# Kernel tuning notes

Measured on AMD Instinct MI355X. Metric: run time of the kernel, lower is better.

## Reference

```python
import jax, jax.numpy as jnp
import numpy as np

EMBED_DIM = 512
NUM_HEADS = 8
HEAD_DIM = EMBED_DIM // NUM_HEADS
PAIR_DIM = 64
B, L = 2, 1024


def setup_inputs() -> dict:
    key = jax.random.key(0)
    ks = jax.random.split(key, 6)
    seq_repr = jax.random.normal(ks[0], (B, L, EMBED_DIM), dtype=jnp.float32)
    pair_repr = jax.random.normal(ks[1], (B, L, L, PAIR_DIM), dtype=jnp.float32)
    # Parameters (stored as [in, out] for x @ W)
    sc = 0.02
    W_qkv = jax.random.normal(ks[2], (EMBED_DIM, 3 * EMBED_DIM), dtype=jnp.float32) * sc
    W_bias = jax.random.normal(ks[3], (PAIR_DIM, NUM_HEADS), dtype=jnp.float32) * sc
    W_out = jax.random.normal(ks[4], (EMBED_DIM, EMBED_DIM), dtype=jnp.float32) * sc
    b_out = jax.random.normal(ks[5], (EMBED_DIM,), dtype=jnp.float32) * sc
    return {"seq_repr": seq_repr, "pair_repr": pair_repr,
            "W_qkv": W_qkv, "W_bias": W_bias, "W_out": W_out, "b_out": b_out}


def reference(seq_repr, pair_repr, W_qkv, W_bias, W_out, b_out):
    b, l, _ = seq_repr.shape
    # pair bias: [B, L, L, pair_dim] -> [B, H, L, L]
    pair_bias = jnp.einsum('bijp,ph->bhij', pair_repr, W_bias)
    qkv = seq_repr @ W_qkv                      # [B, L, 3*E]
    q, k, v = jnp.split(qkv, 3, axis=-1)
    def heads(x):
        return x.reshape(b, l, NUM_HEADS, HEAD_DIM).transpose(0, 2, 1, 3)  # [B,H,L,D]
    q, k, v = heads(q), heads(k), heads(v)
    scale = 1.0 / jnp.sqrt(jnp.asarray(HEAD_DIM, dtype=q.dtype))
    scores = jnp.einsum('bhid,bhjd->bhij', q, k) * scale + pair_bias
    attn = jax.nn.softmax(scores, axis=-1)
    ctx = jnp.einsum('bhij,bhjd->bhid', attn, v)             # [B,H,L,D]
    ctx = ctx.transpose(0, 2, 1, 3).reshape(b, l, EMBED_DIM)
    return ctx @ W_out + b_out
```

## Files before the change

kernel.cpp:

```cpp
#include <hip/hip_runtime.h>
#include <hip/hip_bf16.h>


typedef __attribute__((ext_vector_type(8))) short bf16x8;
typedef __attribute__((ext_vector_type(4))) float f32x4;

#define BFLO(u) __uint_as_float(((unsigned)(u)) << 16)

__device__ __forceinline__ unsigned pk2(float a, float b) {
    __hip_bfloat16 ha = __float2bfloat16(a);
    __hip_bfloat16 hb = __float2bfloat16(b);
    return (unsigned)__bfloat16_as_ushort(ha) | ((unsigned)__bfloat16_as_ushort(hb) << 16);
}

__device__ __forceinline__ void gl16_nt(const void* g, void* l) {
    __builtin_amdgcn_global_load_lds((const __attribute__((address_space(1))) void*)g,
                                     (__attribute__((address_space(3))) void*)l, 16, 0, 2);
}

__global__ __launch_bounds__(256) void prep_kernel(
    const float* __restrict__ seq, const float* __restrict__ W,
    unsigned short* __restrict__ seqb, unsigned short* __restrict__ wtb)
{
    __shared__ float T[64 * 68];
    const int bx = blockIdx.x, t = threadIdx.x;
    if (bx < 512) {
        const size_t idx = ((size_t)bx * 256 + t) * 8;
        float4 f0 = *(const float4*)&seq[idx];
        float4 f1 = *(const float4*)&seq[idx + 4];
        uint4 u;
        u.x = pk2(f0.x, f0.y); u.y = pk2(f0.z, f0.w);
        u.z = pk2(f1.x, f1.y); u.w = pk2(f1.z, f1.w);
        *(uint4*)&seqb[idx] = u;
    } else {
        const int bb = bx - 512;
        const int n0 = (bb % 24) * 64, k0 = (bb / 24) * 64;
        const int kk = t >> 2, nch = (t & 3) * 16;
#pragma unroll
        for (int u = 0; u < 4; u++) {
            float4 f = *(const float4*)&W[(size_t)(k0 + kk) * 1536 + n0 + nch + u * 4];
            T[kk * 68 + nch + u * 4 + 0] = f.x;
            T[kk * 68 + nch + u * 4 + 1] = f.y;
            T[kk * 68 + nch + u * 4 + 2] = f.z;
            T[kk * 68 + nch + u * 4 + 3] = f.w;
        }
        __syncthreads();
        const int nn = t >> 2, kch = (t & 3) * 16;
#pragma unroll
        for (int u = 0; u < 4; u++) {
            float a = T[(kch + u * 4 + 0) * 68 + nn];
            float b = T[(kch + u * 4 + 1) * 68 + nn];
            float c = T[(kch + u * 4 + 2) * 68 + nn];
            float d = T[(kch + u * 4 + 3) * 68 + nn];
            uint2 p; p.x = pk2(a, b); p.y = pk2(c, d);
            *(uint2*)&wtb[(size_t)(n0 + nn) * 512 + k0 + kch + u * 4] = p;
        }
    }
}

__global__ __launch_bounds__(256) void gemm_qkv_kernel(
    const unsigned short* __restrict__ seqb, const unsigned short* __restrict__ wtb,
    unsigned short* __restrict__ qbus, unsigned short* __restrict__ kbus,
    unsigned short* __restrict__ vtbus)
{
    const int t    = threadIdx.x;
    const int lane = t & 63;
    const int wv   = t >> 6;
    const int q4   = lane >> 4;
    const int l15  = lane & 15;
    const int mw   = wv >> 1, nw = wv & 1;

    const int m0 = blockIdx.y * 64;
    const int n0 = blockIdx.x * 64;

    f32x4 acc[2][2];
#pragma unroll
    for (int a = 0; a < 2; a++)
#pragma unroll
        for (int b = 0; b < 2; b++) acc[a][b] = (f32x4){0.f, 0.f, 0.f, 0.f};

    const unsigned short* arow0 = seqb + (size_t)(m0 + mw * 32 + l15) * 512 + q4 * 8;
    const unsigned short* brow0 = wtb + (size_t)(n0 + nw * 32 + l15) * 512 + q4 * 8;

#pragma unroll 4
    for (int k0 = 0; k0 < 512; k0 += 32) {
        uint4 af[2], bf[2];
        af[0] = *(const uint4*)(arow0 + k0);
        af[1] = *(const uint4*)(arow0 + 16 * 512 + k0);
        bf[0] = *(const uint4*)(brow0 + k0);
        bf[1] = *(const uint4*)(brow0 + 16 * 512 + k0);
#pragma unroll
        for (int sm = 0; sm < 2; sm++)
#pragma unroll
            for (int sn = 0; sn < 2; sn++)
                acc[sm][sn] = __builtin_amdgcn_mfma_f32_16x16x32_bf16(
                    *(bf16x8*)&af[sm], *(bf16x8*)&bf[sn], acc[sm][sn], 0, 0, 0);
    }

    const int sect = n0 >> 9;
    const int h    = (n0 >> 6) & 7;
    const int b    = m0 >> 10;
    const int i0   = m0 & 1023;

#pragma unroll
    for (int sm = 0; sm < 2; sm++) {
#pragma unroll
        for (int sn = 0; sn < 2; sn++) {
            const int d  = nw * 32 + sn * 16 + l15;
            const int ib = i0 + mw * 32 + sm * 16 + q4 * 4;
            if (sect == 2) {
                uint2 p;
                p.x = pk2(acc[sm][sn][0], acc[sm][sn][1]);
                p.y = pk2(acc[sm][sn][2], acc[sm][sn][3]);
                *(uint2*)&vtbus[(((size_t)(b * 8 + h)) * 64 + d) * 1024 + ib] = p;
            } else {
                unsigned short* dst = (sect == 0) ? qbus : kbus;
                const float sc = (sect == 0) ? 0.125f : 1.0f;
#pragma unroll
                for (int rr = 0; rr < 4; rr++)
                    dst[(((size_t)(b * 8 + h)) * 1024 + ib + rr) * 64 + d] =
                        __bfloat16_as_ushort(__float2bfloat16(acc[sm][sn][rr] * sc));
            }
        }
    }
}

__device__ __forceinline__ bf16x8 slab_frag(const char* rowb, int ks, int q4, int sw) {
    const int s0 = ks * 8 + q4 * 2;
    const float4 fa = *(const float4*)(rowb + (((s0    ) ^ sw) << 4));
    const float4 fb = *(const float4*)(rowb + (((s0 + 1) ^ sw) << 4));
    uint4 u;
    u.x = pk2(fa.x, fa.y); u.y = pk2(fa.z, fa.w);
    u.z = pk2(fb.x, fb.y); u.w = pk2(fb.z, fb.w);
    return *(bf16x8*)&u;
}

__global__ __launch_bounds__(512, 4) void attn_kernel(
    const float* __restrict__ pair, const float* __restrict__ Wb,
    const unsigned short* __restrict__ qbus, const unsigned short* __restrict__ kbus,
    const unsigned short* __restrict__ vtbus, float* __restrict__ cp,
    float* __restrict__ mlm, float* __restrict__ mll)
{
    __shared__ __align__(16) char plds[2][32768];
    __shared__ __align__(16) unsigned short bias_lds[2][128 * 17];
    __shared__ __align__(16) unsigned short pbuf[8 * 16 * 24];

    const int t    = threadIdx.x;
    const int lane = t & 63;
    const int w    = t >> 6;
    const int q4   = lane >> 4;
    const int l15  = lane & 15;

    const int bx   = blockIdx.x;
    const int vbid = ((bx & 7) << 6) | (bx >> 3);
    const int b    = vbid >> 8;
    const int rem  = vbid & 255;
    const int jh   = rem >> 7;
    const int i0   = (rem & 127) * 8;

    uint4 wbf[2];
#pragma unroll
    for (int ks = 0; ks < 2; ks++) {
        float f[8];
#pragma unroll
        for (int e = 0; e < 8; e++)
            f[e] = (l15 < 8) ? Wb[(ks * 32 + q4 * 8 + e) * 8 + l15] : 0.f;
        wbf[ks].x = pk2(f[0], f[1]); wbf[ks].y = pk2(f[2], f[3]);
        wbf[ks].z = pk2(f[4], f[5]); wbf[ks].w = pk2(f[6], f[7]);
    }

    uint4 qf[2] = {};
    if (l15 < 8) {
        const unsigned short* qrow = qbus + (size_t)((b * 8 + w) * 1024 + i0 + l15) * 64;
#pragma unroll
        for (int ks = 0; ks < 2; ks++)
            qf[ks] = *(const uint4*)(qrow + ks * 32 + q4 * 8);
    }

    asm volatile("s_waitcnt vmcnt(0)" ::: "memory");
    __builtin_amdgcn_sched_barrier(0);

    const char* prow = (const char*)pair
                     + ((size_t)(b * 1024 + i0 + w) * 1024 + jh * 512) * 256;
    int soff[4];
#pragma unroll
    for (int r = 0; r < 4; r++) {
        const int jl = r * 4 + q4;
        soff[r] = jl * 256 + ((l15 ^ jl) << 4);
    }
    char* ldsW = (char*)plds + w * 4096;

#define STAGE(bufsel, jtn) do {                                         \
        const char* gg = prow + (size_t)(jtn) * 4096;                   \
        char* ld = ldsW + (bufsel) * 32768;                             \
        _Pragma("unroll")                                               \
        for (int r = 0; r < 4; r++)                                     \
            gl16_nt(gg + soff[r], ld + r * 1024);                       \
    } while (0)

#define BIASCOMP(pbsel, slot) do {                                      \
        const char* rowb = (const char*)plds + (pbsel) * 32768          \
                         + w * 4096 + l15 * 256;                        \
        f32x4 bb = {0.f, 0.f, 0.f, 0.f};                                \
        _Pragma("unroll")                                               \
        for (int ks = 0; ks < 2; ks++)                                  \
            bb = __builtin_amdgcn_mfma_f32_16x16x32_bf16(               \
                    slab_frag(rowb, ks, q4, l15), *(bf16x8*)&wbf[ks],   \
                    bb, 0, 0, 0);                                       \
        if (l15 < 8) {                                                  \
            _Pragma("unroll")                                           \
            for (int rr = 0; rr < 4; rr++)                              \
                bias_lds[slot][(w * 16 + q4 * 4 + rr) * 17 + l15] =     \
                    __bfloat16_as_ushort(__float2bfloat16(bb[rr]));     \
        }                                                               \
    } while (0)

    STAGE(0, 0);
    STAGE(1, 1);
    asm volatile("s_waitcnt vmcnt(4)" ::: "memory");
    __builtin_amdgcn_sched_barrier(0);
    BIASCOMP(0, 0);
    asm volatile("s_waitcnt lgkmcnt(0)" ::: "memory");
    __builtin_amdgcn_sched_barrier(0);
    __builtin_amdgcn_s_barrier();
    __builtin_amdgcn_sched_barrier(0);

    f32x4 acc[4];
#pragma unroll
    for (int dn = 0; dn < 4; dn++) acc[dn] = (f32x4){0.f, 0.f, 0.f, 0.f};
    float mrun[4], lrun[4];
#pragma unroll
    for (int rr = 0; rr < 4; rr++) { mrun[rr] = -3.0e38f; lrun[rr] = 0.f; }

    const unsigned short* kbase = kbus + (size_t)((b * 8 + w) * 1024 + jh * 512) * 64;
    const unsigned short* vbase = vtbus + (size_t)((b * 8 + w) * 64) * 1024 + jh * 512;

#pragma unroll 1
    for (int jt = 0; jt < 32; jt++) {
        uint4 kf[2], vf[4];
        {
            const unsigned short* kt = kbase + (size_t)(jt * 16 + l15) * 64;
            kf[0] = *(const uint4*)(kt + q4 * 8);
            kf[1] = *(const uint4*)(kt + 32 + q4 * 8);
#pragma unroll
            for (int dn = 0; dn < 4; dn++)
                vf[dn] = *(const uint4*)(vbase + (size_t)(dn * 16 + l15) * 1024
                                         + jt * 16 + (q4 & 1) * 8);
        }

        if (jt < 30) {
            STAGE(jt & 1, jt + 2);
            asm volatile("s_waitcnt vmcnt(10)" ::: "memory");
            __builtin_amdgcn_sched_barrier(0);
            BIASCOMP((jt + 1) & 1, (jt + 1) & 1);
        } else if (jt == 30) {
            asm volatile("s_waitcnt vmcnt(6)" ::: "memory");
            __builtin_amdgcn_sched_barrier(0);
            BIASCOMP(1, 1);
        }

        f32x4 s;
#pragma unroll
        for (int rr = 0; rr < 4; rr++) {
            const int ii = q4 * 4 + rr;
            s[rr] = (q4 < 2) ? BFLO(bias_lds[jt & 1][(ii * 16 + l15) * 17 + w]) : 0.f;
        }
        s = __builtin_amdgcn_mfma_f32_16x16x32_bf16(*(bf16x8*)&qf[0], *(bf16x8*)&kf[0], s, 0, 0, 0);
        s = __builtin_amdgcn_mfma_f32_16x16x32_bf16(*(bf16x8*)&qf[1], *(bf16x8*)&kf[1], s, 0, 0, 0);

#pragma unroll
        for (int rr = 0; rr < 4; rr++) {
            float x = s[rr];
            x = fmaxf(x, __shfl_xor(x, 1));
            x = fmaxf(x, __shfl_xor(x, 2));
            x = fmaxf(x, __shfl_xor(x, 4));
            x = fmaxf(x, __shfl_xor(x, 8));
            const float mnew = fmaxf(mrun[rr], x);
            const float corr = __expf(mrun[rr] - mnew);
            mrun[rr] = mnew;
            const float p0 = __expf(s[rr] - mnew);
            float ts = p0;
            ts += __shfl_xor(ts, 1);
            ts += __shfl_xor(ts, 2);
            ts += __shfl_xor(ts, 4);
            ts += __shfl_xor(ts, 8);
            lrun[rr] = lrun[rr] * corr + ts;
#pragma unroll
            for (int dn = 0; dn < 4; dn++) acc[dn][rr] *= corr;
            pbuf[(w * 16 + q4 * 4 + rr) * 24 + l15] =
                __bfloat16_as_ushort(__float2bfloat16(p0));
        }

        asm volatile("s_waitcnt lgkmcnt(0)" ::: "memory");
        __builtin_amdgcn_sched_barrier(0);

        bf16x8 pfrag = (bf16x8){0, 0, 0, 0, 0, 0, 0, 0};
        if (q4 < 2) pfrag = *(bf16x8*)&pbuf[(w * 16 + l15) * 24 + q4 * 8];
#pragma unroll
        for (int dn = 0; dn < 4; dn++)
            acc[dn] = __builtin_amdgcn_mfma_f32_16x16x32_bf16(pfrag, *(bf16x8*)&vf[dn], acc[dn], 0, 0, 0);

        asm volatile("s_waitcnt lgkmcnt(0)" ::: "memory");
        __builtin_amdgcn_sched_barrier(0);
        __builtin_amdgcn_s_barrier();
        __builtin_amdgcn_sched_barrier(0);
    }

    if (q4 < 2) {
#pragma unroll
        for (int rr = 0; rr < 4; rr++) {
            const int i = q4 * 4 + rr;
            float* crow = cp + (size_t)jh * (2048 * 512)
                        + ((size_t)(b * 1024) + i0 + i) * 512 + w * 64;
#pragma unroll
            for (int dn = 0; dn < 4; dn++)
                crow[dn * 16 + l15] = acc[dn][rr];
            if (l15 == 0) {
                const int mi = ((jh * 2 + b) * 8 + w) * 1024 + i0 + i;
                mlm[mi] = mrun[rr];
                mll[mi] = lrun[rr];
            }
        }
    }
#undef STAGE
#undef BIASCOMP
}

__global__ __launch_bounds__(256, 2) void gemm_out_fused(
    const float* __restrict__ cp, const float* __restrict__ mlm,
    const float* __restrict__ mll, const float* __restrict__ W,
    const float* __restrict__ bias, float* __restrict__ out)
{
    __shared__ float smem[64 * 68];
    float* As = smem;
    float* Bs = smem + 32 * 68;

    const int t  = threadIdx.x;
    const int m0 = blockIdx.y * 64;
    const int n0 = blockIdx.x * 64;
    const int tx = t & 15, ty = t >> 4;

    const int am = t >> 2, ak = (t & 3) * 8;
    const int bk = t >> 3, bn = (t & 7) * 8;

    const int row = m0 + am;
    const int bb  = row >> 10, ii = row & 1023;
    const float* cp0 = cp + (size_t)row * 512;
    const float* cp1 = cp + (size_t)(2048 * 512) + (size_t)row * 512;

    float acc[4][4] = {};
    float w0 = 0.f, w1 = 0.f;

    for (int k0 = 0; k0 < 512; k0 += 32) {
        if ((k0 & 63) == 0) {
            const int h   = k0 >> 6;
            const int mi0 = ((bb) * 8 + h) * 1024 + ii;
            const int mi1 = ((2 + bb) * 8 + h) * 1024 + ii;
            const float m0_ = mlm[mi0], m1_ = mlm[mi1];
            const float l0_ = mll[mi0], l1_ = mll[mi1];
            const float M   = fmaxf(m0_, m1_);
            float e0 = __expf(m0_ - M), e1 = __expf(m1_ - M);
            const float inv = 1.0f / (l0_ * e0 + l1_ * e1);
            w0 = e0 * inv; w1 = e1 * inv;
        }
        float4 c0a = *(const float4*)&cp0[k0 + ak];
        float4 c0b = *(const float4*)&cp0[k0 + ak + 4];
        float4 c1a = *(const float4*)&cp1[k0 + ak];
        float4 c1b = *(const float4*)&cp1[k0 + ak + 4];
        float4 b0 = *(const float4*)&W[(size_t)(k0 + bk) * 512 + n0 + bn];
        float4 b1 = *(const float4*)&W[(size_t)(k0 + bk) * 512 + n0 + bn + 4];
        float a0x = c0a.x * w0 + c1a.x * w1, a0y = c0a.y * w0 + c1a.y * w1;
        float a0z = c0a.z * w0 + c1a.z * w1, a0w = c0a.w * w0 + c1a.w * w1;
        float a1x = c0b.x * w0 + c1b.x * w1, a1y = c0b.y * w0 + c1b.y * w1;
        float a1z = c0b.z * w0 + c1b.z * w1, a1w = c0b.w * w0 + c1b.w * w1;
        __syncthreads();
        As[(ak + 0) * 68 + am] = a0x;
        As[(ak + 1) * 68 + am] = a0y;
        As[(ak + 2) * 68 + am] = a0z;
        As[(ak + 3) * 68 + am] = a0w;
        As[(ak + 4) * 68 + am] = a1x;
        As[(ak + 5) * 68 + am] = a1y;
        As[(ak + 6) * 68 + am] = a1z;
        As[(ak + 7) * 68 + am] = a1w;
        *(float4*)&Bs[bk * 68 + bn]     = b0;
        *(float4*)&Bs[bk * 68 + bn + 4] = b1;
        __syncthreads();
#pragma unroll
        for (int kk = 0; kk < 32; kk++) {
            float4 a4 = *(float4*)&As[kk * 68 + ty * 4];
            float4 b4 = *(float4*)&Bs[kk * 68 + tx * 4];
            float av[4] = {a4.x, a4.y, a4.z, a4.w};
            float bv[4] = {b4.x, b4.y, b4.z, b4.w};
#pragma unroll
            for (int r = 0; r < 4; r++)
#pragma unroll
                for (int c = 0; c < 4; c++) acc[r][c] += av[r] * bv[c];
        }
    }

    float4 bo = *(const float4*)&bias[n0 + tx * 4];
    float bv[4] = {bo.x, bo.y, bo.z, bo.w};
#pragma unroll
    for (int r = 0; r < 4; r++) {
        const int m = m0 + ty * 4 + r;
#pragma unroll
        for (int c = 0; c < 4; c++)
            out[(size_t)m * 512 + n0 + tx * 4 + c] = acc[r][c] + bv[c];
    }
}

extern "C" void kernel_launch(void* const* d_in, const int* in_sizes, int n_in,
                              void* d_out, int out_size, void* d_ws, size_t ws_size,
                              hipStream_t stream)
{
    const float* seq  = (const float*)d_in[0];
    const float* pair = (const float*)d_in[1];
    const float* Wqkv = (const float*)d_in[2];
    const float* Wb   = (const float*)d_in[3];
    const float* Wout = (const float*)d_in[4];
    const float* bout = (const float*)d_in[5];
    float* out = (float*)d_out;

    unsigned short* qbus  = (unsigned short*)d_ws;
    unsigned short* kbus  = qbus + (1 << 20);
    unsigned short* vtbus = kbus + (1 << 20);
    unsigned short* seqb  = vtbus + (1 << 20);
    unsigned short* wtb   = seqb + (1 << 20);
    float*          cp    = (float*)(wtb + (1 << 20));
    float*          mlm   = cp + (2 << 20);
    float*          mll   = mlm + (1 << 15);

    prep_kernel<<<704, 256, 0, stream>>>(seq, Wqkv, seqb, wtb);
    gemm_qkv_kernel<<<dim3(24, 32), 256, 0, stream>>>(seqb, wtb, qbus, kbus, vtbus);
    attn_kernel<<<512, 512, 0, stream>>>(pair, Wb, qbus, kbus, vtbus, cp, mlm, mll);
    gemm_out_fused<<<dim3(8, 32), 256, 0, stream>>>(cp, mlm, mll, Wout, bout, out);
}
```

Measured before the change: 232.9 us.

## Split pair-bias projection into a separate kernel writing bf16 bias

Moves the pair_repr × W_bias projection out of the attention kernel into a standalone streaming kernel that writes a bf16 [B,H,L,L] bias tensor, which attention then reads per tile. This removes the LDS double-buffered pair staging and the per-iteration block barrier from the attention loop. In exchange it adds a kernel launch and an extra 32 MB of bf16 bias written and read back through global memory.

```diff
diff --git a/kernel.cpp b/kernel.cpp
--- a/kernel.cpp
+++ b/kernel.cpp
@@ -4,6 +4,7 @@
 
 typedef __attribute__((ext_vector_type(8))) short bf16x8;
 typedef __attribute__((ext_vector_type(4))) float f32x4;
+typedef __attribute__((ext_vector_type(4))) unsigned int u32x4;
 
 #define BFLO(u) __uint_as_float(((unsigned)(u)) << 16)
 
@@ -11,11 +12,6 @@
     __hip_bfloat16 ha = __float2bfloat16(a);
     __hip_bfloat16 hb = __float2bfloat16(b);
     return (unsigned)__bfloat16_as_ushort(ha) | ((unsigned)__bfloat16_as_ushort(hb) << 16);
-}
-
-__device__ __forceinline__ void gl16_nt(const void* g, void* l) {
-    __builtin_amdgcn_global_load_lds((const __attribute__((address_space(1))) void*)g,
-                                     (__attribute__((address_space(3))) void*)l, 16, 0, 2);
 }
 
 __global__ __launch_bounds__(256) void prep_kernel(
@@ -125,24 +121,78 @@
     }
 }
 
-__device__ __forceinline__ bf16x8 slab_frag(const char* rowb, int ks, int q4, int sw) {
-    const int s0 = ks * 8 + q4 * 2;
-    const float4 fa = *(const float4*)(rowb + (((s0    ) ^ sw) << 4));
-    const float4 fb = *(const float4*)(rowb + (((s0 + 1) ^ sw) << 4));
-    uint4 u;
-    u.x = pk2(fa.x, fa.y); u.y = pk2(fa.z, fa.w);
-    u.z = pk2(fb.x, fb.y); u.w = pk2(fb.z, fb.w);
-    return *(bf16x8*)&u;
+__global__ __launch_bounds__(256) void bias_kernel(
+    const float* __restrict__ pair, const float* __restrict__ Wb,
+    unsigned short* __restrict__ biasb)
+{
+    const int t    = threadIdx.x;
+    const int lane = t & 63;
+    const int wv   = t >> 6;
+    const int q4   = lane >> 4;
+    const int l15  = lane & 15;
+
+    uint4 wbf[2];
+#pragma unroll
+    for (int ks = 0; ks < 2; ks++) {
+        float f[8];
+#pragma unroll
+        for (int e = 0; e < 8; e++)
+            f[e] = (l15 < 8) ? Wb[(ks * 32 + q4 * 8 + e) * 8 + l15] : 0.f;
+        wbf[ks].x = pk2(f[0], f[1]); wbf[ks].y = pk2(f[2], f[3]);
+        wbf[ks].z = pk2(f[4], f[5]); wbf[ks].w = pk2(f[6], f[7]);
+    }
+
+    const int u = blockIdx.x * 4 + wv;
+    const size_t r0base = (size_t)u * 256;
+    const float* rp0 = pair + (r0base + l15) * 64;
+
+    u32x4 pf[2][4];
+#define LOADG(ph, g) do {                                                     \
+        const float* rp = rp0 + (size_t)(g) * 16 * 64;                        \
+        _Pragma("unroll")                                                     \
+        for (int ld = 0; ld < 4; ld++)                                        \
+            pf[ph][ld] = __builtin_nontemporal_load(                          \
+                (const u32x4*)(rp + (ld >> 1) * 32 + q4 * 8 + (ld & 1) * 4)); \
+    } while (0)
+
+    LOADG(0, 0);
+
+#pragma unroll 1
+    for (int g = 0; g < 16; g++) {
+        if (g < 15) LOADG((g + 1) & 1, g + 1);
+
+        const int ph = g & 1;
+        f32x4 c = {0.f, 0.f, 0.f, 0.f};
+#pragma unroll
+        for (int ks = 0; ks < 2; ks++) {
+            float4 fa = *(float4*)&pf[ph][ks * 2];
+            float4 fb = *(float4*)&pf[ph][ks * 2 + 1];
+            uint4 af;
+            af.x = pk2(fa.x, fa.y); af.y = pk2(fa.z, fa.w);
+            af.z = pk2(fb.x, fb.y); af.w = pk2(fb.z, fb.w);
+            c = __builtin_amdgcn_mfma_f32_16x16x32_bf16(*(bf16x8*)&af, *(bf16x8*)&wbf[ks], c, 0, 0, 0);
+        }
+
+        if (l15 < 8) {
+            const size_t r0 = r0base + (size_t)g * 16;
+            const int b   = (int)(r0 >> 20);
+            const int i   = (int)((r0 >> 10) & 1023);
+            const int j0g = (int)(r0 & 1023);
+            unsigned short* dp = biasb + ((((size_t)(b * 8 + l15)) * 1024 + i) << 10)
+                               + j0g + q4 * 4;
+            *(unsigned*)dp       = pk2(c[0], c[1]);
+            *(unsigned*)(dp + 2) = pk2(c[2], c[3]);
+        }
+    }
+#undef LOADG
 }
 
 __global__ __launch_bounds__(512, 4) void attn_kernel(
-    const float* __restrict__ pair, const float* __restrict__ Wb,
-    const unsigned short* __restrict__ qbus, const unsigned short* __restrict__ kbus,
-    const unsigned short* __restrict__ vtbus, float* __restrict__ cp,
-    float* __restrict__ mlm, float* __restrict__ mll)
-{
-    __shared__ __align__(16) char plds[2][32768];
-    __shared__ __align__(16) unsigned short bias_lds[2][128 * 17];
+    const unsigned short* __restrict__ biasb, const unsigned short* __restrict__ qbus,
+    const unsigned short* __restrict__ kbus, const unsigned short* __restrict__ vtbus,
+    float* __restrict__ cp, float* __restrict__ mlm, float* __restrict__ mll)
+{
+    __shared__ __align__(8) unsigned short lbias[8][8][16];
     __shared__ __align__(16) unsigned short pbuf[8 * 16 * 24];
 
     const int t    = threadIdx.x;
@@ -158,17 +208,6 @@
     const int jh   = rem >> 7;
     const int i0   = (rem & 127) * 8;
 
-    uint4 wbf[2];
-#pragma unroll
-    for (int ks = 0; ks < 2; ks++) {
-        float f[8];
-#pragma unroll
-        for (int e = 0; e < 8; e++)
-            f[e] = (l15 < 8) ? Wb[(ks * 32 + q4 * 8 + e) * 8 + l15] : 0.f;
-        wbf[ks].x = pk2(f[0], f[1]); wbf[ks].y = pk2(f[2], f[3]);
-        wbf[ks].z = pk2(f[4], f[5]); wbf[ks].w = pk2(f[6], f[7]);
-    }
-
     uint4 qf[2] = {};
     if (l15 < 8) {
         const unsigned short* qrow = qbus + (size_t)((b * 8 + w) * 1024 + i0 + l15) * 64;
@@ -177,53 +216,12 @@
             qf[ks] = *(const uint4*)(qrow + ks * 32 + q4 * 8);
     }
 
-    asm volatile("s_waitcnt vmcnt(0)" ::: "memory");
-    __builtin_amdgcn_sched_barrier(0);
-
-    const char* prow = (const char*)pair
-                     + ((size_t)(b * 1024 + i0 + w) * 1024 + jh * 512) * 256;
-    int soff[4];
-#pragma unroll
-    for (int r = 0; r < 4; r++) {
-        const int jl = r * 4 + q4;
-        soff[r] = jl * 256 + ((l15 ^ jl) << 4);
-    }
-    char* ldsW = (char*)plds + w * 4096;
-
-#define STAGE(bufsel, jtn) do {                                         \
-        const char* gg = prow + (size_t)(jtn) * 4096;                   \
-        char* ld = ldsW + (bufsel) * 32768;                             \
-        _Pragma("unroll")                                               \
-        for (int r = 0; r < 4; r++)                                     \
-            gl16_nt(gg + soff[r], ld + r * 1024);                       \
-    } while (0)
-
-#define BIASCOMP(pbsel, slot) do {                                      \
-        const char* rowb = (const char*)plds + (pbsel) * 32768          \
-                         + w * 4096 + l15 * 256;                        \
-        f32x4 bb = {0.f, 0.f, 0.f, 0.f};                                \
-        _Pragma("unroll")                                               \
-        for (int ks = 0; ks < 2; ks++)                                  \
-            bb = __builtin_amdgcn_mfma_f32_16x16x32_bf16(               \
-                    slab_frag(rowb, ks, q4, l15), *(bf16x8*)&wbf[ks],   \
-                    bb, 0, 0, 0);                                       \
-        if (l15 < 8) {                                                  \
-            _Pragma("unroll")                                           \
-            for (int rr = 0; rr < 4; rr++)                              \
-                bias_lds[slot][(w * 16 + q4 * 4 + rr) * 17 + l15] =     \
-                    __bfloat16_as_ushort(__float2bfloat16(bb[rr]));     \
-        }                                                               \
-    } while (0)
-
-    STAGE(0, 0);
-    STAGE(1, 1);
-    asm volatile("s_waitcnt vmcnt(4)" ::: "memory");
-    __builtin_amdgcn_sched_barrier(0);
-    BIASCOMP(0, 0);
-    asm volatile("s_waitcnt lgkmcnt(0)" ::: "memory");
-    __builtin_amdgcn_sched_barrier(0);
-    __builtin_amdgcn_s_barrier();
-    __builtin_amdgcn_sched_barrier(0);
+    const int brow = (lane >> 2) & 7;
+    const int bjq  = lane & 3;
+    const unsigned short* bB = biasb
+        + ((size_t)((b * 8 + w) * 1024) + i0 + brow) * 1024 + jh * 512 + bjq * 4;
+
+    uint2 breg = *(const uint2*)bB;
 
     f32x4 acc[4];
 #pragma unroll
@@ -248,23 +246,17 @@
                                          + jt * 16 + (q4 & 1) * 8);
         }
 
-        if (jt < 30) {
-            STAGE(jt & 1, jt + 2);
-            asm volatile("s_waitcnt vmcnt(10)" ::: "memory");
-            __builtin_amdgcn_sched_barrier(0);
-            BIASCOMP((jt + 1) & 1, (jt + 1) & 1);
-        } else if (jt == 30) {
-            asm volatile("s_waitcnt vmcnt(6)" ::: "memory");
-            __builtin_amdgcn_sched_barrier(0);
-            BIASCOMP(1, 1);
-        }
+        uint2 bnext = breg;
+        if (jt < 31) bnext = *(const uint2*)(bB + (jt + 1) * 16);
+
+        if (lane < 32) *(uint2*)&lbias[w][brow][bjq * 4] = breg;
+        asm volatile("s_waitcnt lgkmcnt(0)" ::: "memory");
+        __builtin_amdgcn_sched_barrier(0);
 
         f32x4 s;
 #pragma unroll
-        for (int rr = 0; rr < 4; rr++) {
-            const int ii = q4 * 4 + rr;
-            s[rr] = (q4 < 2) ? BFLO(bias_lds[jt & 1][(ii * 16 + l15) * 17 + w]) : 0.f;
-        }
+        for (int rr = 0; rr < 4; rr++)
+            s[rr] = (q4 < 2) ? BFLO(lbias[w][q4 * 4 + rr][l15]) : 0.f;
         s = __builtin_amdgcn_mfma_f32_16x16x32_bf16(*(bf16x8*)&qf[0], *(bf16x8*)&kf[0], s, 0, 0, 0);
         s = __builtin_amdgcn_mfma_f32_16x16x32_bf16(*(bf16x8*)&qf[1], *(bf16x8*)&kf[1], s, 0, 0, 0);
 
@@ -300,10 +292,7 @@
         for (int dn = 0; dn < 4; dn++)
             acc[dn] = __builtin_amdgcn_mfma_f32_16x16x32_bf16(pfrag, *(bf16x8*)&vf[dn], acc[dn], 0, 0, 0);
 
-        asm volatile("s_waitcnt lgkmcnt(0)" ::: "memory");
-        __builtin_amdgcn_sched_barrier(0);
-        __builtin_amdgcn_s_barrier();
-        __builtin_amdgcn_sched_barrier(0);
+        breg = bnext;
     }
 
     if (q4 < 2) {
@@ -322,8 +311,6 @@
             }
         }
     }
-#undef STAGE
-#undef BIASCOMP
 }
 
 __global__ __launch_bounds__(256, 2) void gemm_out_fused(
@@ -429,9 +416,11 @@
     float*          cp    = (float*)(wtb + (1 << 20));
     float*          mlm   = cp + (2 << 20);
     float*          mll   = mlm + (1 << 15);
+    unsigned short* biasb = (unsigned short*)(mll + (1 << 15));
 
     prep_kernel<<<704, 256, 0, stream>>>(seq, Wqkv, seqb, wtb);
     gemm_qkv_kernel<<<dim3(24, 32), 256, 0, stream>>>(seqb, wtb, qbus, kbus, vtbus);
-    attn_kernel<<<512, 512, 0, stream>>>(pair, Wb, qbus, kbus, vtbus, cp, mlm, mll);
+    bias_kernel<<<2048, 256, 0, stream>>>(pair, Wb, biasb);
+    attn_kernel<<<512, 512, 0, stream>>>(biasb, qbus, kbus, vtbus, cp, mlm, mll);
     gemm_out_fused<<<dim3(8, 32), 256, 0, stream>>>(cp, mlm, mll, Wout, bout, out);
 }
```

Result: slower. 295.5 us (+26.9%).
